# Performance work log

Hardware: AMD Instinct MI355X
Metric: run time of the kernel (lower is better)

## Reference

```python
import jax, jax.numpy as jnp
import numpy as np
import math

B, T, C_IN = 4, 2048, 1024
HIDDEN, HEADS = 1024, 8
HEAD_DIM = HIDDEN // HEADS
OUT_DIM = 1024
EPS = 1e-8


def setup_inputs() -> dict:
    key = jax.random.key(0)
    ks = jax.random.split(key, 12)
    s_in = 1.0 / math.sqrt(C_IN)
    s_h = 1.0 / math.sqrt(HIDDEN)
    x = jax.random.normal(ks[0], (B, T, C_IN), dtype=jnp.float32)
    # causal keep-mask (True = keep), broadcast over batch
    attn_mask = jnp.broadcast_to(jnp.tril(jnp.ones((T, T), dtype=bool)), (B, T, T))
    Wu = jax.random.normal(ks[1], (HIDDEN, C_IN), dtype=jnp.float32) * s_in
    bu = jnp.zeros((HIDDEN,), dtype=jnp.float32)
    Wv = jax.random.normal(ks[2], (HIDDEN, C_IN), dtype=jnp.float32) * s_in
    bv = jnp.zeros((HIDDEN,), dtype=jnp.float32)
    Wq = jax.random.normal(ks[3], (HIDDEN, C_IN), dtype=jnp.float32) * s_in
    bq = jnp.zeros((HIDDEN,), dtype=jnp.float32)
    Wk = jax.random.normal(ks[4], (HIDDEN, C_IN), dtype=jnp.float32) * s_in
    bk = jnp.zeros((HIDDEN,), dtype=jnp.float32)
    Wf = jax.random.normal(ks[5], (OUT_DIM, HIDDEN), dtype=jnp.float32) * s_h
    bf = jnp.zeros((OUT_DIM,), dtype=jnp.float32)
    g_norm = jnp.ones((HIDDEN,), dtype=jnp.float32)
    return {"x": x, "attn_mask": attn_mask, "Wu": Wu, "bu": bu, "Wv": Wv,
            "bv": bv, "Wq": Wq, "bq": bq, "Wk": Wk, "bk": bk,
            "Wf": Wf, "bf": bf, "g_norm": g_norm}


def _heads(t):  # (B,T,HIDDEN) -> (B,H,T,D)
    b, s, _ = t.shape
    return t.reshape(b, s, HEADS, HEAD_DIM).transpose(0, 2, 1, 3)


def reference(x, attn_mask, Wu, bu, Wv, bv, Wq, bq, Wk, bk, Wf, bf, g_norm):
    silu = jax.nn.silu
    U = silu(x @ Wu.T + bu)
    V = silu(x @ Wv.T + bv)
    Q = silu(x @ Wq.T + bq)
    K = silu(x @ Wk.T + bk)
    Qh, Kh, Vh = _heads(Q), _heads(K), _heads(V)
    scale = 1.0 / math.sqrt(HEAD_DIM)
    logits = jnp.einsum('bhtd,bhsd->bhts', Qh, Kh) * scale
    A = jnp.maximum(silu(logits), 0.0)
    A = jnp.where(attn_mask[:, None, :, :], A, 0.0)
    denom = A.sum(axis=-1, keepdims=True)
    A = jnp.where(denom > 1e-12, A / (denom + EPS), 0.0)
    AVh = jnp.einsum('bhts,bhsd->bhtd', A, Vh)
    AV = AVh.transpose(0, 2, 1, 3).reshape(x.shape[0], x.shape[1], HIDDEN)
    # RMSNorm (torch nn.RMSNorm default eps = dtype eps)
    rms_eps = jnp.finfo(AV.dtype).eps
    AV_norm = AV * jax.lax.rsqrt(jnp.mean(AV * AV, axis=-1, keepdims=True) + rms_eps) * g_norm
    UV = AV_norm * U
    return UV @ Wf.T + bf
```

## Files before the change

### kernel.cpp

```cpp
#include <hip/hip_runtime.h>
#include <hip/hip_bf16.h>
#include <stdint.h>

#define Tlen  2048
#define M_TOK 8192

typedef __attribute__((ext_vector_type(8))) __bf16 bf16x8;
typedef __attribute__((ext_vector_type(4))) float  f32x4;
typedef unsigned short u16;
typedef unsigned int   u32;
typedef unsigned long long u64;

__device__ __forceinline__ float b2f(u16 u) {
  union { float f; u32 i; } v; v.i = ((u32)u) << 16; return v.f;
}
__device__ __forceinline__ u16 f2b(float f) {
  u32 x = __float_as_uint(f);
  return (u16)((x + 0x7FFFu + ((x >> 16) & 1u)) >> 16);
}
__device__ __forceinline__ u32 f2b2(float lo, float hi) {
  __hip_bfloat162 h = __float22bfloat162_rn(float2{lo, hi});
  return *reinterpret_cast<u32*>(&h);
}
__device__ __forceinline__ bf16x8 ld8(const u16* p) {
  return *reinterpret_cast<const bf16x8*>(p);
}
__device__ __forceinline__ bool probe_bf16(const void* g) {
  return *(const u32*)g == 0x3F803F80u;
}
__device__ __forceinline__ void stage8(u16* dst, const void* src, size_t eidx, bool isbf) {
  if (isbf) {
    *(uint4*)dst = *(const uint4*)((const u16*)src + eidx);
  } else {
    const float* f = (const float*)src + eidx;
    float4 a = *(const float4*)f;
    float4 b = *(const float4*)(f + 4);
    u32 t[4] = { f2b2(a.x, a.y), f2b2(a.z, a.w), f2b2(b.x, b.y), f2b2(b.z, b.w) };
    *(uint4*)dst = *(uint4*)t;
  }
}
__device__ __forceinline__ void gl_lds16(const void* g, void* l) {
  __builtin_amdgcn_global_load_lds(
      (const __attribute__((address_space(1))) u32*)g,
      (__attribute__((address_space(3))) u32*)l, 16, 0, 0);
}
__device__ __forceinline__ int swz128(int r, int c) {
  return r * 128 + ((((c >> 3) ^ (r & 15))) << 3) + (c & 7);
}

__global__ __launch_bounds__(256) void prep1(
    const void* __restrict__ x,
    const void* __restrict__ Wu, const void* __restrict__ Wv,
    const void* __restrict__ Wq, const void* __restrict__ Wk,
    const void* __restrict__ bu, const void* __restrict__ bv,
    const void* __restrict__ bq, const void* __restrict__ bk,
    u16* __restrict__ xb, u16* __restrict__ Wcat, u16* __restrict__ bcat,
    const void* __restrict__ gprobe)
{
  const bool isbf = probe_bf16(gprobe);
  long i = (long)blockIdx.x * 256 + threadIdx.x;
  if (i < 1048576) { stage8(&xb[i * 8], x, (size_t)i * 8, isbf); return; }
  i -= 1048576;
  if (i < 524288) {
    int w = (int)(i >> 17); long e = i & 131071;
    const void* s = (w == 0) ? Wu : (w == 1) ? Wv : (w == 2) ? Wq : Wk;
    stage8(&Wcat[((size_t)w << 20) + e * 8], s, (size_t)e * 8, isbf); return;
  }
  i -= 524288;
  if (i < 512) {
    int w = (int)(i >> 7); int e = (int)(i & 127);
    const void* s = (w == 0) ? bu : (w == 1) ? bv : (w == 2) ? bq : bk;
    stage8(&bcat[w * 1024 + e * 8], s, (size_t)e * 8, isbf);
  }
}

__global__ __launch_bounds__(256) void prep2(
    const void* __restrict__ Wf, const void* __restrict__ bf_,
    u16* __restrict__ Wfb, u16* __restrict__ bfb,
    const void* __restrict__ gprobe)
{
  const bool isbf = probe_bf16(gprobe);
  long i = (long)blockIdx.x * 256 + threadIdx.x;
  if (i < 131072) { stage8(&Wfb[i * 8], Wf, (size_t)i * 8, isbf); return; }
  i -= 131072;
  if (i < 128) stage8(&bfb[i * 8], bf_, (size_t)i * 8, isbf);
}

__global__ __launch_bounds__(512, 2) void gemm_proj(
    const u16* __restrict__ X,
    const u16* __restrict__ W,
    const u16* __restrict__ bias,
    u16* __restrict__ U, u16* __restrict__ Vt,
    u16* __restrict__ Qb, u16* __restrict__ Kb)
{
  __shared__ __align__(16) u16 SMEM[65536];
  const int tid  = threadIdx.x;
  const int lane = tid & 63;
  const int wave = tid >> 6;
  const int wm   = wave >> 2;
  const int wn   = wave & 3;
  const int l15  = lane & 15;
  const int quad = lane >> 4;

  const int id = ((blockIdx.x & 7) << 6) | (blockIdx.x >> 3);
  const int by = id >> 4;
  const int bx = id & 15;
  const int m0 = by << 8;
  const int n0 = bx << 8;

  const int slotoff = (l15 * 4 + quad) * 8;
  const u16* Xsrc = X + (size_t)(m0 + wave * 32 + (lane >> 2)) * 1024 + ((lane & 3) << 3);
  const u16* Wsrc = W + (size_t)(n0 + wave * 32 + (lane >> 2)) * 1024 + ((lane & 3) << 3);
  const int ldsw = wave << 10;

  bf16x8 a[4], b[4];
  f32x4 acc[8][4] = {};

#define BAR() __builtin_amdgcn_s_barrier()
#define WAITV(n) asm volatile("s_waitcnt vmcnt(" #n ")" ::: "memory")
#define STAGE_A(t, kh, sbuf) do { \
    const int _kb = ((t) << 6) + ((kh) << 5); \
    u16* _l = &SMEM[((sbuf) << 14) + ((kh) << 13) + ldsw]; \
    gl_lds16(Xsrc + _kb, _l); \
    gl_lds16(Xsrc + 16384 + _kb, _l + 512); \
  } while (0)
#define STAGE_B(t, kh, sbuf) do { \
    const int _kb = ((t) << 6) + ((kh) << 5); \
    u16* _l = &SMEM[32768 + ((sbuf) << 14) + ((kh) << 13) + ldsw]; \
    gl_lds16(Wsrc + _kb, _l); \
    gl_lds16(Wsrc + 16384 + _kb, _l + 512); \
  } while (0)
#define LDA(h, kh, sbuf) do { \
    const u16* _p = &SMEM[((sbuf) << 14) + ((kh) << 13) + ((wm * 8 + (h) * 4) << 9) + slotoff]; \
    a[0] = ld8(_p); a[1] = ld8(_p + 512); a[2] = ld8(_p + 1024); a[3] = ld8(_p + 1536); \
  } while (0)
#define LDB(kh, sbuf) do { \
    const u16* _p = &SMEM[32768 + ((sbuf) << 14) + ((kh) << 13) + ((wn * 4) << 9) + slotoff]; \
    b[0] = ld8(_p); b[1] = ld8(_p + 512); b[2] = ld8(_p + 1024); b[3] = ld8(_p + 1536); \
  } while (0)
#define MFMA16(h) do { \
    __builtin_amdgcn_s_setprio(1); \
    _Pragma("unroll") \
    for (int _mt = 0; _mt < 4; _mt++) { \
      _Pragma("unroll") \
      for (int _nt = 0; _nt < 4; _nt++) \
        acc[(h) * 4 + _mt][_nt] = __builtin_amdgcn_mfma_f32_16x16x32_bf16( \
            a[_mt], b[_nt], acc[(h) * 4 + _mt][_nt], 0, 0, 0); \
    } \
    __builtin_amdgcn_s_setprio(0); \
  } while (0)

  STAGE_A(0, 0, 0); STAGE_B(0, 0, 0); STAGE_A(0, 1, 0); STAGE_B(0, 1, 0);
  WAITV(4);
  STAGE_A(1, 0, 1); STAGE_B(1, 0, 1); STAGE_A(1, 1, 1);
  WAITV(6);
  BAR();

#define GROUP(t, buf) do { \
    LDA(0, 0, buf); LDB(0, buf); STAGE_B((t) + 1, 1, (buf) ^ 1); \
    BAR(); MFMA16(0); BAR(); \
    LDA(1, 0, buf); STAGE_A((t) + 2, 0, buf); \
    BAR(); MFMA16(1); BAR(); \
    LDA(0, 1, buf); LDB(1, buf); STAGE_B((t) + 2, 0, buf); \
    BAR(); MFMA16(0); BAR(); \
    LDA(1, 1, buf); STAGE_A((t) + 2, 1, buf); \
    BAR(); MFMA16(1); WAITV(6); BAR(); \
  } while (0)

#pragma unroll 1
  for (int u = 0; u < 14; u += 2) {
    GROUP(u, 0);
    GROUP(u + 1, 1);
  }
  LDA(0, 0, 0); LDB(0, 0); STAGE_B(15, 1, 1);
  BAR(); MFMA16(0); BAR();
  LDA(1, 0, 0);
  BAR(); MFMA16(1); BAR();
  LDA(0, 1, 0); LDB(1, 0);
  BAR(); MFMA16(0); BAR();
  LDA(1, 1, 0);
  BAR(); MFMA16(1); WAITV(0); BAR();
  LDA(0, 0, 1); LDB(0, 1); MFMA16(0);
  LDA(1, 0, 1); MFMA16(1);
  LDA(0, 1, 1); LDB(1, 1); MFMA16(0);
  LDA(1, 1, 1); MFMA16(1);

#undef GROUP
#undef MFMA16
#undef LDB
#undef LDA
#undef STAGE_B
#undef STAGE_A
#undef WAITV
#undef BAR

  const int grp = bx >> 2;

  if (grp != 1) {
    u16* dst = (grp == 0) ? U : (grp == 2) ? Qb : Kb;
    const float postmul = (grp == 3) ? 0.08838834764831845f : 1.0f;
#pragma unroll
    for (int nt = 0; nt < 4; nt++) {
      const int ng = n0 + wn * 64 + nt * 16 + l15;
      const float bv = b2f(bias[ng]);
      const int ncol = ng & 1023;
#pragma unroll
      for (int fm = 0; fm < 8; fm++) {
#pragma unroll
        for (int r = 0; r < 4; r++) {
          const int m = m0 + wm * 128 + fm * 16 + quad * 4 + r;
          float v = acc[fm][nt][r] + bv;
          v = v * __builtin_amdgcn_rcpf(1.0f + __expf(-v));
          dst[(size_t)m * 1024 + ncol] = f2b(v * postmul);
        }
      }
    }
    return;
  }

  u16* Ls = SMEM;
  const int hb  = (n0 & 1023) >> 7;
  const int bh0 = (m0 >> 11) * 8;
  const int t0  = m0 & 2047;
#pragma unroll
  for (int pass = 0; pass < 2; pass++) {
    __syncthreads();
    if (wm == pass) {
#pragma unroll
      for (int nt = 0; nt < 4; nt++) {
        const int ng = n0 + wn * 64 + nt * 16 + l15;
        const float bv = b2f(bias[ng]);
        const int rowl = wn * 64 + nt * 16 + l15;
#pragma unroll
        for (int fm = 0; fm < 8; fm++) {
          float vv[4];
#pragma unroll
          for (int r = 0; r < 4; r++) {
            float v = acc[fm][nt][r] + bv;
            vv[r] = v * __builtin_amdgcn_rcpf(1.0f + __expf(-v));
          }
          const int coll = fm * 16 + quad * 4;
          u64 pk = (u64)f2b2(vv[0], vv[1]) | ((u64)f2b2(vv[2], vv[3]) << 32);
          *(u64*)&Ls[swz128(rowl, coll)] = pk;
        }
      }
    }
    __syncthreads();
    const int rr = tid & 255;
    const int c0 = tid >> 8;
#pragma unroll
    for (int p = 0; p < 8; p++) {
      const int chunk = c0 + p * 2;
      uint4 vv4 = *(const uint4*)&Ls[swz128(rr, chunk * 8)];
      *(uint4*)&Vt[((size_t)(bh0 + hb + (rr >> 7)) * 128 + (rr & 127)) * 2048
                   + t0 + pass * 128 + chunk * 8] = vv4;
    }
  }
}

__global__ __launch_bounds__(256) void gemm_final(
    const u16* __restrict__ X,
    const u16* __restrict__ W,
    const u16* __restrict__ bias,
    float* __restrict__ O)
{
  __shared__ u16 Xs[128 * 64];
  __shared__ u16 Ws[64 * 64];
  const int tid  = threadIdx.x;
  const int lane = tid & 63;
  const int wave = tid >> 6;
  const int l15  = lane & 15;
  const int quad = lane >> 4;
  const int m0 = blockIdx.y * 128;
  const int n0 = blockIdx.x * 64;

  const int ro = lane >> 3;
  const int ch = lane & 7;
  const int cc = ch ^ ro;

  f32x4 acc[2][4] = {};

  for (int k0 = 0; k0 < 1024; k0 += 64) {
    __syncthreads();
#pragma unroll
    for (int j = 0; j < 4; j++) {
      int r0 = wave * 32 + j * 8;
      gl_lds16(X + (size_t)(m0 + r0 + ro) * 1024 + k0 + cc * 8, &Xs[r0 * 64]);
    }
#pragma unroll
    for (int j = 0; j < 2; j++) {
      int r0 = wave * 16 + j * 8;
      gl_lds16(W + (size_t)(n0 + r0 + ro) * 1024 + k0 + cc * 8, &Ws[r0 * 64]);
    }
    __syncthreads();

#pragma unroll
    for (int kk = 0; kk < 64; kk += 32) {
      bf16x8 a[2], b[4];
      const int g = (kk >> 3) + quad;
      const int lch = (g ^ (l15 & 7)) << 3;
#pragma unroll
      for (int mt = 0; mt < 2; mt++)
        a[mt] = ld8(&Xs[(wave * 32 + mt * 16 + l15) * 64 + lch]);
#pragma unroll
      for (int nt = 0; nt < 4; nt++)
        b[nt] = ld8(&Ws[(nt * 16 + l15) * 64 + lch]);
#pragma unroll
      for (int mt = 0; mt < 2; mt++)
#pragma unroll
        for (int nt = 0; nt < 4; nt++)
          acc[mt][nt] = __builtin_amdgcn_mfma_f32_16x16x32_bf16(a[mt], b[nt], acc[mt][nt], 0, 0, 0);
    }
  }

#pragma unroll
  for (int nt = 0; nt < 4; nt++) {
    int n = n0 + nt * 16 + l15;
    float bv = b2f(bias[n]);
#pragma unroll
    for (int mt = 0; mt < 2; mt++)
#pragma unroll
      for (int r = 0; r < 4; r++) {
        int m = m0 + wave * 32 + mt * 16 + quad * 4 + r;
        O[(size_t)m * 1024 + n] = acc[mt][nt][r] + bv;
      }
  }
}

__global__ __launch_bounds__(256, 4) void attn_kernel(
    const u16* __restrict__ Q,
    const u16* __restrict__ K,
    const u16* __restrict__ Vt,
    u16* __restrict__ AV)
{
  __shared__ u16 Ks[64 * 128];
  __shared__ u16 Vts[128 * 64];
  u16* As = Ks;

  const int tid  = threadIdx.x;
  const int lane = tid & 63;
  const int wave = tid >> 6;
  const int l15  = lane & 15;
  const int quad = lane >> 4;
  const int qt = 31 - (blockIdx.x >> 5);
  const int bh = blockIdx.x & 31;
  const int q0 = qt * 64;
  const size_t rowbase = (size_t)(bh >> 3) * Tlen;
  const int cbase = (bh & 7) * 128;
  const size_t vbase = (size_t)bh * 128 * 2048;
  const int mrow = wave * 16;

  bf16x8 bq[4];
#pragma unroll
  for (int kk = 0; kk < 4; kk++)
    bq[kk] = ld8(&Q[(rowbase + q0 + mrow + l15) * 1024 + cbase + kk * 32 + quad * 8]);

  f32x4 avacc[8] = {};
  float denom = 0.f;
  const int t_abs = q0 + mrow + l15;

  for (int s0 = 0; s0 <= q0; s0 += 64) {
    __syncthreads();
    {
      const int ro16 = lane >> 4, ch16 = lane & 15;
#pragma unroll
      for (int j = 0; j < 4; j++) {
        int r0 = wave * 16 + j * 4;
        int cc = ch16 ^ ((r0 + ro16) & 15);
        gl_lds16(&K[(rowbase + s0 + r0 + ro16) * 1024 + cbase + cc * 8], &Ks[r0 * 128]);
      }
      const int ro8 = lane >> 3, ch8 = lane & 7;
#pragma unroll
      for (int j = 0; j < 4; j++) {
        int d0 = wave * 32 + j * 8;
        int cc = ch8 ^ ((d0 + ro8) & 7);
        gl_lds16(&Vt[vbase + (size_t)(d0 + ro8) * 2048 + s0 + cc * 8], &Vts[d0 * 64]);
      }
    }
    __syncthreads();

    f32x4 sacc[4] = {};
#pragma unroll
    for (int kk = 0; kk < 4; kk++) {
      bf16x8 a[4];
      const int lch = (((kk * 4) + quad) ^ l15) << 3;
#pragma unroll
      for (int nt = 0; nt < 4; nt++)
        a[nt] = ld8(&Ks[(nt * 16 + l15) * 128 + lch]);
#pragma unroll
      for (int nt = 0; nt < 4; nt++)
        sacc[nt] = __builtin_amdgcn_mfma_f32_16x16x32_bf16(a[nt], bq[kk], sacc[nt], 0, 0, 0);
    }
    __syncthreads();

    const bool maskneed = (s0 + 63 > q0 + mrow);
    float rs = 0.f;
#pragma unroll
    for (int nt = 0; nt < 4; nt++) {
      float aa[4];
#pragma unroll
      for (int r = 0; r < 4; r++) {
        int s_abs = s0 + nt * 16 + quad * 4 + r;
        float z = sacc[nt][r];
        float a = fmaxf(z, 0.f) * __builtin_amdgcn_rcpf(1.0f + __expf(-z));
        if (maskneed && (s_abs > t_abs)) a = 0.0f;
        rs += a;
        aa[r] = a;
      }
      u64 pk = (u64)f2b2(aa[0], aa[1]) | ((u64)f2b2(aa[2], aa[3]) << 32);
      *(u64*)&As[(mrow + l15) * 72 + nt * 16 + quad * 4] = pk;
    }
    rs += __shfl_xor(rs, 16);
    rs += __shfl_xor(rs, 32);
    denom += rs;

#pragma unroll
    for (int kk = 0; kk < 2; kk++) {
      bf16x8 a, b[8];
      const int lch8 = (((kk * 4) + quad) ^ (l15 & 7)) << 3;
      a = ld8(&As[(mrow + l15) * 72 + kk * 32 + quad * 8]);
#pragma unroll
      for (int dt = 0; dt < 8; dt++)
        b[dt] = ld8(&Vts[(dt * 16 + l15) * 64 + lch8]);
#pragma unroll
      for (int dt = 0; dt < 8; dt++)
        avacc[dt] = __builtin_amdgcn_mfma_f32_16x16x32_bf16(a, b[dt], avacc[dt], 0, 0, 0);
    }
  }

  __syncthreads();
  u16* Ls = Ks;
#pragma unroll
  for (int r = 0; r < 4; r++) {
    float dn = __shfl(denom, (lane & 48) | (quad * 4 + r));
    float sc = (dn > 1e-12f) ? __builtin_amdgcn_rcpf(dn + 1e-8f) : 0.0f;
    int rl = mrow + quad * 4 + r;
#pragma unroll
    for (int dt = 0; dt < 8; dt++)
      Ls[swz128(rl, dt * 16 + l15)] = f2b(avacc[dt][r] * sc);
  }
  __syncthreads();

  const int rr = tid & 63;
  const int c0 = tid >> 6;
#pragma unroll
  for (int p = 0; p < 4; p++) {
    int chunk = c0 + p * 4;
    uint4 vv = *(const uint4*)&Ls[swz128(rr, chunk * 8)];
    *(uint4*)&AV[(rowbase + q0 + rr) * 1024 + cbase + chunk * 8] = vv;
  }
}

__global__ __launch_bounds__(256) void rms_mul(
    const u16* __restrict__ AV, const u16* __restrict__ U,
    const void* __restrict__ g, u16* __restrict__ Y)
{
  const bool isbf = probe_bf16(g);
  const int row = blockIdx.x;
  const int tid = threadIdx.x;
  const size_t base = (size_t)row * 1024;
  uint2 pav = *(const uint2*)&AV[base + tid * 4];
  const u16* pe = (const u16*)&pav;
  float v[4];
  float ss = 0.f;
#pragma unroll
  for (int j = 0; j < 4; j++) { v[j] = b2f(pe[j]); ss += v[j] * v[j]; }
#pragma unroll
  for (int m = 1; m < 64; m <<= 1) ss += __shfl_xor(ss, m);
  __shared__ float red[4];
  if ((tid & 63) == 0) red[tid >> 6] = ss;
  __syncthreads();
  float tot = red[0] + red[1] + red[2] + red[3];
  float rinv = rsqrtf(tot * (1.0f / 1024.0f) + 1.1920929e-7f);
  uint2 pu = *(const uint2*)&U[base + tid * 4];
  const u16* ue = (const u16*)&pu;
  u16 out4[4];
#pragma unroll
  for (int j = 0; j < 4; j++) {
    float gj = isbf ? b2f(((const u16*)g)[tid * 4 + j]) : ((const float*)g)[tid * 4 + j];
    out4[j] = f2b(v[j] * rinv * gj * b2f(ue[j]));
  }
  *(uint2*)&Y[base + tid * 4] = *(uint2*)out4;
}

extern "C" void kernel_launch(void* const* d_in, const int* in_sizes, int n_in,
                              void* d_out, int out_size, void* d_ws, size_t ws_size,
                              hipStream_t stream)
{
  (void)in_sizes; (void)out_size; (void)ws_size;
  const int off = (n_in >= 13) ? 0 : -1;
  const void* x   = d_in[0];
  const void* Wu  = d_in[2 + off];
  const void* bu  = d_in[3 + off];
  const void* Wv  = d_in[4 + off];
  const void* bv  = d_in[5 + off];
  const void* Wq  = d_in[6 + off];
  const void* bq  = d_in[7 + off];
  const void* Wk  = d_in[8 + off];
  const void* bk  = d_in[9 + off];
  const void* Wf  = d_in[10 + off];
  const void* bf_ = d_in[11 + off];
  const void* gn  = d_in[12 + off];

  const size_t NELT = (size_t)M_TOK * 1024;
  u16* xb  = (u16*)d_ws;
  u16* U   = xb + NELT;
  u16* Vt  = U  + NELT;
  u16* Qb  = Vt + NELT;
  u16* Kb  = Qb + NELT;
  u16* AVb = Qb;
  u16* Y   = Kb;
  u16* Wfb = xb;
  u16* bfb = xb + (size_t)1024 * 1024;

  u16* Wcat = (u16*)d_out;
  u16* bcat = Wcat + (size_t)4096 * 1024;

  prep1<<<dim3(6146), 256, 0, stream>>>(x, Wu, Wv, Wq, Wk, bu, bv, bq, bk,
                                        xb, Wcat, bcat, gn);

  gemm_proj<<<dim3(512), 512, 0, stream>>>(xb, Wcat, bcat, U, Vt, Qb, Kb);

  prep2<<<dim3(513), 256, 0, stream>>>(Wf, bf_, Wfb, bfb, gn);

  attn_kernel<<<dim3(1024), 256, 0, stream>>>(Qb, Kb, Vt, AVb);
  rms_mul<<<dim3(M_TOK), 256, 0, stream>>>(AVb, U, gn, Y);

  gemm_final<<<dim3(16, 64), 256, 0, stream>>>(Y, Wfb, bfb, (float*)d_out);
}
```

Measured before the change: 338.2 us.

## Restructure GEMM global-to-LDS staging order and lane mapping in projection kernel

Changes the lane-to-row mapping of the direct global-to-LDS loads so each lane reads a contiguous slot (slotoff = lane*8), with 16 rows by 4 column chunks per wave. Reorders the prefetch schedule so A and B half-tiles for the same k-half are staged together, with more vmcnt waits and barriers spread through the group. The tail is also reworked to add barriers between the final MFMA phases. The aim is better-balanced load issue and less stalling in the projection GEMM, at the cost of extra waits and barriers and a different global access pattern (16 rows per instruction, 64B per row) that could coalesce worse.

```diff
diff --git a/kernel.cpp b/kernel.cpp
--- a/kernel.cpp
+++ b/kernel.cpp
@@ -108,9 +108,9 @@
   const int m0 = by << 8;
   const int n0 = bx << 8;
 
-  const int slotoff = (l15 * 4 + quad) * 8;
-  const u16* Xsrc = X + (size_t)(m0 + wave * 32 + (lane >> 2)) * 1024 + ((lane & 3) << 3);
-  const u16* Wsrc = W + (size_t)(n0 + wave * 32 + (lane >> 2)) * 1024 + ((lane & 3) << 3);
+  const int slotoff = lane * 8;
+  const u16* Xsrc = X + (size_t)(m0 + wave * 32 + (lane & 15)) * 1024 + ((lane >> 4) << 3);
+  const u16* Wsrc = W + (size_t)(n0 + wave * 32 + (lane & 15)) * 1024 + ((lane >> 4) << 3);
   const int ldsw = wave << 10;
 
   bf16x8 a[4], b[4];
@@ -150,21 +150,22 @@
     __builtin_amdgcn_s_setprio(0); \
   } while (0)
 
-  STAGE_A(0, 0, 0); STAGE_B(0, 0, 0); STAGE_A(0, 1, 0); STAGE_B(0, 1, 0);
-  WAITV(4);
-  STAGE_A(1, 0, 1); STAGE_B(1, 0, 1); STAGE_A(1, 1, 1);
-  WAITV(6);
+  STAGE_A(0, 0, 0); STAGE_B(0, 0, 0);
+  STAGE_A(0, 1, 0); STAGE_B(0, 1, 0);
+  STAGE_A(1, 0, 1); STAGE_B(1, 0, 1);
+  WAITV(8);
   BAR();
 
 #define GROUP(t, buf) do { \
-    LDA(0, 0, buf); LDB(0, buf); STAGE_B((t) + 1, 1, (buf) ^ 1); \
+    LDA(0, 0, buf); LDB(0, buf); STAGE_A((t) + 1, 1, (buf) ^ 1); STAGE_B((t) + 1, 1, (buf) ^ 1); \
     BAR(); MFMA16(0); BAR(); \
-    LDA(1, 0, buf); STAGE_A((t) + 2, 0, buf); \
+    LDA(1, 0, buf); \
     BAR(); MFMA16(1); BAR(); \
-    LDA(0, 1, buf); LDB(1, buf); STAGE_B((t) + 2, 0, buf); \
+    WAITV(8); \
+    LDA(0, 1, buf); LDB(1, buf); STAGE_A((t) + 2, 0, buf); STAGE_B((t) + 2, 0, buf); \
     BAR(); MFMA16(0); BAR(); \
-    LDA(1, 1, buf); STAGE_A((t) + 2, 1, buf); \
-    BAR(); MFMA16(1); WAITV(6); BAR(); \
+    LDA(1, 1, buf); \
+    BAR(); MFMA16(1); WAITV(8); BAR(); \
   } while (0)
 
 #pragma unroll 1
@@ -172,18 +173,24 @@
     GROUP(u, 0);
     GROUP(u + 1, 1);
   }
-  LDA(0, 0, 0); LDB(0, 0); STAGE_B(15, 1, 1);
+  LDA(0, 0, 0); LDB(0, 0); STAGE_A(15, 1, 1); STAGE_B(15, 1, 1);
   BAR(); MFMA16(0); BAR();
   LDA(1, 0, 0);
   BAR(); MFMA16(1); BAR();
+  WAITV(8);
   LDA(0, 1, 0); LDB(1, 0);
   BAR(); MFMA16(0); BAR();
   LDA(1, 1, 0);
-  BAR(); MFMA16(1); WAITV(0); BAR();
-  LDA(0, 0, 1); LDB(0, 1); MFMA16(0);
-  LDA(1, 0, 1); MFMA16(1);
-  LDA(0, 1, 1); LDB(1, 1); MFMA16(0);
-  LDA(1, 1, 1); MFMA16(1);
+  BAR(); MFMA16(1); WAITV(4); BAR();
+  LDA(0, 0, 1); LDB(0, 1);
+  BAR(); MFMA16(0); BAR();
+  LDA(1, 0, 1);
+  BAR(); MFMA16(1); BAR();
+  WAITV(0);
+  LDA(0, 1, 1); LDB(1, 1);
+  BAR(); MFMA16(0); BAR();
+  LDA(1, 1, 1);
+  MFMA16(1);
 
 #undef GROUP
 #undef MFMA16
```

New measurement: 357.5 us. 1.06x slower.
